# Optimization experiments

Hardware: AMD Instinct MI355X
Metric: run time of the kernel (lower is better)

The kernel has to match this reference:

```python
import jax, jax.numpy as jnp
import numpy as np
from jax import lax

EPS = 1e-5  # BatchNorm eps (inference mode: running_mean=m, running_var=v)
DN = ('NCDHW', 'OIDHW', 'NCDHW')


def _conv_bn_relu(x, W, b, g, bt, m, v, pad):
    y = lax.conv_general_dilated(x, W, window_strides=(1, 1, 1), padding=pad,
                                 dimension_numbers=DN)
    y = y + b[None, :, None, None, None]
    scale = g / jnp.sqrt(v + EPS)
    y = (y - m[None, :, None, None, None]) * scale[None, :, None, None, None] \
        + bt[None, :, None, None, None]
    return jax.nn.relu(y)


def _cal_patt(k, q, v):
    # spatial non-local attention over H*W, independently per (n, c, d)
    N, C, D, H, W = q.shape
    qf = q.reshape(N, C, D, H * W)
    kf = k.reshape(N, C, D, H * W)
    vf = v.reshape(N, C, D, H * W)
    # sigma[n,c,d,i,j] = q_i * k_j ; softmax over j ; out[j] = sum_i v_i * r_ij
    sigma = qf[..., :, None] * kf[..., None, :]          # [N,C,D,HW,HW]
    r = jax.nn.softmax(sigma, axis=-1)
    out = jnp.einsum('ncdi,ncdij->ncdj', vf, r)
    return out.reshape(N, C, D, H, W)


def _cal_datt(k, q, v):
    # temporal non-local attention over D, independently per (n, c, h, w)
    N, C, D, H, W = q.shape
    qf = jnp.transpose(q, (0, 1, 3, 4, 2))               # [N,C,H,W,D]
    kf = jnp.transpose(k, (0, 1, 3, 4, 2))
    vf = jnp.transpose(v, (0, 1, 3, 4, 2))
    sigma = qf[..., :, None] * kf[..., None, :]          # [N,C,H,W,D,D]
    r = jax.nn.softmax(sigma, axis=-1)
    out = jnp.einsum('nchwi,nchwij->nchwj', vf, r)
    return jnp.transpose(out, (0, 1, 4, 2, 3))           # back to [N,C,D,H,W]


def setup_inputs() -> dict:
    key = jax.random.key(0)
    ks = jax.random.split(key, 8)
    C, Cc = 512, 64  # features_, features_//compress
    N, D, H, W = 2, 8, 16, 16
    f32 = jnp.float32

    def bn(c):
        return (jnp.ones((c,), f32), jnp.zeros((c,), f32),
                jnp.zeros((c,), f32), jnp.ones((c,), f32))

    x = jax.random.normal(ks[0], (N, C, D, H, W), f32)
    Wq = jax.random.normal(ks[1], (Cc, C, 1, 1, 1), f32) * 0.04
    Wk = jax.random.normal(ks[2], (Cc, C, 1, 1, 1), f32) * 0.04
    Wv = jax.random.normal(ks[3], (Cc, C, 1, 1, 1), f32) * 0.04
    Ws = jax.random.normal(ks[4], (C, Cc, 3, 3, 3), f32) * 0.02
    Wd = jax.random.normal(ks[5], (C, Cc, 3, 3, 3), f32) * 0.02
    gq, btq, mq, vq = bn(Cc)
    gk, btk, mk, vk = bn(Cc)
    gv, btv, mv, vv = bn(Cc)
    gs, bts, ms, vs = bn(C)
    gd, btd, md, vd = bn(C)
    return dict(
        x=x, gama=jnp.float32(0.5),
        Wq=Wq, bq=jnp.zeros((Cc,), f32), gq=gq, btq=btq, mq=mq, vq=vq,
        Wk=Wk, bk=jnp.zeros((Cc,), f32), gk=gk, btk=btk, mk=mk, vk=vk,
        Wv=Wv, bv=jnp.zeros((Cc,), f32), gv=gv, btv=btv, mv=mv, vv=vv,
        Ws=Ws, bs=jnp.zeros((C,), f32), gs=gs, bts=bts, ms=ms, vs=vs,
        Wd=Wd, bd=jnp.zeros((C,), f32), gd=gd, btd=btd, md=md, vd=vd,
    )


def reference(x, gama,
              Wq, bq, gq, btq, mq, vq,
              Wk, bk, gk, btk, mk, vk,
              Wv, bv, gv, btv, mv, vv,
              Ws, bs, gs, bts, ms, vs,
              Wd, bd, gd, btd, md, vd):
    P0 = [(0, 0)] * 3
    P1 = [(1, 1)] * 3
    v_x = _conv_bn_relu(x, Wv, bv, gv, btv, mv, vv, P0)
    k_x = _conv_bn_relu(x, Wk, bk, gk, btk, mk, vk, P0)
    q_x = _conv_bn_relu(x, Wq, bq, gq, btq, mq, vq, P0)
    # name == 'st': both spatial and temporal attention branches
    Patt = _cal_patt(k_x, q_x, v_x)
    Patt_c = _conv_bn_relu(Patt, Ws, bs, gs, bts, ms, vs, P1)
    Datt = _cal_datt(k_x, q_x, v_x)
    Datt_c = _conv_bn_relu(Datt, Wd, bd, gd, btd, md, vd, P1)
    return gama * (Datt_c + Patt_c) + x
```

## Files before the change

### kernel.cpp

```cpp
#include <hip/hip_runtime.h>
#include <cmath>

#define EPSBN 1e-5f

namespace {
constexpr int C_IN = 512;
constexpr int CC   = 64;
constexpr int CD   = 8;
constexpr int HW   = 256;
constexpr int DHW  = CD * HW;
constexpr int QSZ  = 2 * CC * DHW;

constexpr int PG    = 18 * 18;
constexpr int GPLN  = PG * 8;
constexpr int PADSZ = 2 * 10 * 8 * GPLN;
constexpr int WTSZ  = 27 * 512 * 64;
constexpr float LOG2E = 1.44269504088896f;

typedef __attribute__((ext_vector_type(8))) short bf16x8;
typedef __attribute__((ext_vector_type(4))) float f32x4;
typedef __attribute__((ext_vector_type(16))) float f32x16;

typedef unsigned int u32_g __attribute__((address_space(1)));
typedef unsigned int u32_l __attribute__((address_space(3)));

__device__ inline unsigned short f2bf(float f) {
    unsigned u = __float_as_uint(f);
    return (unsigned short)((u + 0x7fffu + ((u >> 16) & 1u)) >> 16);
}
}

__global__ __launch_bounds__(256) void prep_small_kernel(
    const float* __restrict__ Wq, const float* __restrict__ Wk,
    const float* __restrict__ Wv, unsigned short* __restrict__ Wqkv,
    uint4* __restrict__ pads)
{
    int bid = blockIdx.x;
    int t = threadIdx.x;
    if (bid < 192) {
        int co = bid;
        const float* W = co < 64 ? Wq : co < 128 ? Wk : Wv;
        int c = co & 63;
        for (int ci = t; ci < 512; ci += 256)
            Wqkv[(size_t)co * 512 + ci] = f2bf(W[(size_t)c * 512 + ci]);
    } else {
        pads[(bid - 192) * 256 + t] = make_uint4(0, 0, 0, 0);
    }
}

__global__ __launch_bounds__(256) void qkv_gemm_kernel(
    const float* __restrict__ x, const unsigned short* __restrict__ Wqkv,
    const float* __restrict__ bq, const float* __restrict__ gq,
    const float* __restrict__ btq, const float* __restrict__ mq,
    const float* __restrict__ vq,
    const float* __restrict__ bk, const float* __restrict__ gk,
    const float* __restrict__ btk, const float* __restrict__ mk,
    const float* __restrict__ vk,
    const float* __restrict__ bv, const float* __restrict__ gv,
    const float* __restrict__ btv, const float* __restrict__ mv,
    const float* __restrict__ vv,
    float* __restrict__ outq, float* __restrict__ outk, float* __restrict__ outv)
{
    int bid = blockIdx.x;
    int n = bid >> 7, p0 = (bid & 127) * 16;

    __shared__ __align__(16) unsigned short xs[16 * 512];
    int t = threadIdx.x;

    const float* xb = x + ((size_t)n * C_IN) * DHW + p0;
#pragma unroll
    for (int pass = 0; pass < 8; ++pass) {
        int idx = pass * 256 + t;
        int ci = idx >> 2, pq = idx & 3;
        float4 v4 = *reinterpret_cast<const float4*>(xb + (size_t)ci * DHW + pq * 4);
        float arr[4] = {v4.x, v4.y, v4.z, v4.w};
#pragma unroll
        for (int u = 0; u < 4; ++u) {
            int pos = pq * 4 + u;
            int boff = pos * 1024 + ((ci * 2) ^ ((pos & 7) << 4));
            *reinterpret_cast<unsigned short*>(
                reinterpret_cast<char*>(xs) + boff) = f2bf(arr[u]);
        }
    }
    __syncthreads();

    int wid = t >> 6, lane = t & 63;
    int l15 = lane & 15, l4 = lane >> 4;
    int mh = wid * 3;
    int pos = l15;

    bf16x8 bfr[16];
    const char* xsb = reinterpret_cast<const char*>(xs) + pos * 1024;
    int swz = (pos & 7) << 4;
#pragma unroll
    for (int kk = 0; kk < 16; ++kk)
        bfr[kk] = *reinterpret_cast<const bf16x8*>(xsb + ((kk * 64 + l4 * 16) ^ swz));

    f32x4 acc[3];
#pragma unroll
    for (int i = 0; i < 3; ++i) acc[i] = (f32x4){0.f, 0.f, 0.f, 0.f};

#pragma unroll
    for (int i = 0; i < 3; ++i) {
        const unsigned short* wrow =
            Wqkv + ((size_t)(mh + i) * 16 + l15) * 512 + l4 * 8;
#pragma unroll
        for (int kk = 0; kk < 16; ++kk) {
            bf16x8 af = *reinterpret_cast<const bf16x8*>(wrow + kk * 32);
            acc[i] = __builtin_amdgcn_mfma_f32_16x16x32_bf16(af, bfr[kk], acc[i], 0, 0, 0);
        }
    }

#pragma unroll
    for (int i = 0; i < 3; ++i) {
        int mf = mh + i;
        int br = mf >> 2;
        const float* bb  = br == 0 ? bq  : br == 1 ? bk  : bv;
        const float* gg  = br == 0 ? gq  : br == 1 ? gk  : gv;
        const float* bt  = br == 0 ? btq : br == 1 ? btk : btv;
        const float* mm  = br == 0 ? mq  : br == 1 ? mk  : mv;
        const float* vvp = br == 0 ? vq  : br == 1 ? vk  : vv;
        float*       op  = br == 0 ? outq : br == 1 ? outk : outv;
        int cb = (mf & 3) * 16 + l4 * 4;
#pragma unroll
        for (int r = 0; r < 4; ++r) {
            int c = cb + r;
            float s = gg[c] * rsqrtf(vvp[c] + EPSBN);
            float val = (acc[i][r] + bb[c] - mm[c]) * s + bt[c];
            op[((size_t)(n * CC + c)) * DHW + p0 + pos] = fmaxf(val, 0.f);
        }
    }
}

__global__ __launch_bounds__(256) void att_kernel(
    const float* __restrict__ q, const float* __restrict__ k,
    const float* __restrict__ v,
    const float* __restrict__ Ws, const float* __restrict__ Wd,
    const float* __restrict__ bs, const float* __restrict__ gs,
    const float* __restrict__ bts, const float* __restrict__ ms,
    const float* __restrict__ vs,
    const float* __restrict__ bd, const float* __restrict__ gd,
    const float* __restrict__ btd, const float* __restrict__ md,
    const float* __restrict__ vd,
    unsigned short* __restrict__ Pp, unsigned short* __restrict__ Dp,
    unsigned short* __restrict__ Wt, float2* __restrict__ BNc)
{
    __shared__ __align__(16) float sk[256], sq2[256], sw[256];
    __shared__ float red[4];
    int t = threadIdx.x;
    int bid = blockIdx.x;

    if (bid < 1024) {
        int n = bid >> 9, c = (bid >> 3) & 63, d = bid & 7;
        size_t base = (size_t)bid * HW;
        float kt = k[base + t];
        float qt = q[base + t];
        float vt = v[base + t];
        float qt2 = qt * LOG2E;
        sk[t]  = kt;
        sq2[t] = qt2;

        float m = kt;
#pragma unroll
        for (int off = 32; off >= 1; off >>= 1)
            m = fmaxf(m, __shfl_xor(m, off));
        if ((t & 63) == 0) red[t >> 6] = m;
        __syncthreads();
        float kmax = fmaxf(fmaxf(red[0], red[1]), fmaxf(red[2], red[3]));

        float qkm2 = qt2 * kmax;
        float d0 = 0.f, d1 = 0.f, d2 = 0.f, d3 = 0.f;
        const float4* sk4 = reinterpret_cast<const float4*>(sk);
#pragma unroll 8
        for (int j = 0; j < 64; ++j) {
            float4 kk = sk4[j];
            d0 += __builtin_amdgcn_exp2f(fmaf(qt2, kk.x, -qkm2));
            d1 += __builtin_amdgcn_exp2f(fmaf(qt2, kk.y, -qkm2));
            d2 += __builtin_amdgcn_exp2f(fmaf(qt2, kk.z, -qkm2));
            d3 += __builtin_amdgcn_exp2f(fmaf(qt2, kk.w, -qkm2));
        }
        float den = (d0 + d1) + (d2 + d3);
        sw[t] = vt / den;
        __syncthreads();

        float kjm = kt - kmax;
        float o0 = 0.f, o1 = 0.f, o2 = 0.f, o3 = 0.f;
        const float4* sw4 = reinterpret_cast<const float4*>(sw);
        const float4* sq4 = reinterpret_cast<const float4*>(sq2);
#pragma unroll 8
        for (int i = 0; i < 64; ++i) {
            float4 ww = sw4[i];
            float4 qq = sq4[i];
            o0 += ww.x * __builtin_amdgcn_exp2f(qq.x * kjm);
            o1 += ww.y * __builtin_amdgcn_exp2f(qq.y * kjm);
            o2 += ww.z * __builtin_amdgcn_exp2f(qq.z * kjm);
            o3 += ww.w * __builtin_amdgcn_exp2f(qq.w * kjm);
        }
        float o = (o0 + o1) + (o2 + o3);

        int h = t >> 4, w = t & 15;
        size_t dst = ((((size_t)(n * 10 + d + 1) * 8 + (c >> 3)) * PG)
                      + (h + 1) * 18 + (w + 1)) * 8 + (c & 7);
        Pp[dst] = f2bf(o);
    } else if (bid < 1152) {
        int g = (bid - 1024) * 256 + t;
        int nc = g >> 8, hw = g & 255;
        int n = nc >> 6, c = nc & 63;
        size_t base = (size_t)nc * DHW + hw;

        float qv[8], kv[8], vv_[8];
#pragma unroll
        for (int d = 0; d < 8; ++d) {
            qv[d]  = q[base + d * HW];
            kv[d]  = k[base + d * HW];
            vv_[d] = v[base + d * HW];
        }
        float kmax = 0.f;
#pragma unroll
        for (int d = 0; d < 8; ++d) kmax = fmaxf(kmax, kv[d]);

        float wgt[8];
#pragma unroll
        for (int i = 0; i < 8; ++i) {
            float den = 0.f, qkm = qv[i] * kmax;
#pragma unroll
            for (int j = 0; j < 8; ++j)
                den += __expf(fmaf(qv[i], kv[j], -qkm));
            wgt[i] = vv_[i] / den;
        }
        int h = hw >> 4, w = hw & 15;
#pragma unroll
        for (int j = 0; j < 8; ++j) {
            float o = 0.f, kjm = kv[j] - kmax;
#pragma unroll
            for (int i = 0; i < 8; ++i)
                o += wgt[i] * __expf(qv[i] * kjm);
            size_t dst = ((((size_t)(n * 10 + j + 1) * 8 + (c >> 3)) * PG)
                          + (h + 1) * 18 + (w + 1)) * 8 + (c & 7);
            Dp[dst] = f2bf(o);
        }
    } else if (bid < 2176) {
        int b2 = bid - 1152;
        int b  = b2 >> 9;
        int co = b2 & 511;
        const float* W = b ? Wd : Ws;
        int cog = co >> 6, co_l = co & 63;
        int r  = co_l & 31, hi = co_l >> 5;
        unsigned short* o = Wt + (size_t)b * WTSZ;
        for (int k2 = t; k2 < 27 * 64; k2 += 256) {
            int ci  = k2 / 27;
            int tap = k2 - ci * 27;
            int kd = tap / 9, tapk = tap - kd * 9;
            int half = ci >> 5, cl = ci & 31;
            int cig = cl >> 4, ci16 = cl & 15;
            int ks = ci16 >> 3;
            float w = W[(size_t)co * 1728 + k2];
            int chunk = ((cog * 2 + half) * 3 + kd) * 2 + cig;
            int pg = (r * 2 + ks) ^ (r & 7);
            o[(size_t)chunk * 9216 + tapk * 1024 + hi * 512
              + pg * 8 + (ci16 & 7)] = f2bf(w);
        }
    } else {
        int gid = (bid - 2176) * 256 + t;
        if (gid < 1024) {
            int br = gid >> 9, co = gid & 511;
            float s, o;
            if (br == 0) {
                s = gs[co] * rsqrtf(vs[co] + EPSBN);
                o = (bs[co] - ms[co]) * s + bts[co];
            } else {
                s = gd[co] * rsqrtf(vd[co] + EPSBN);
                o = (bd[co] - md[co]) * s + btd[co];
            }
            BNc[gid] = make_float2(s, o);
        }
    }
}

__global__ __launch_bounds__(256, 1) void conv_fused_kernel(
    const unsigned short* __restrict__ Pp, const unsigned short* __restrict__ Dp,
    const unsigned short* __restrict__ Wt,
    const float2* __restrict__ BNc,
    const float* __restrict__ x, const float* __restrict__ gama,
    float* __restrict__ out)
{
    int bid = blockIdx.x;
    int cog = bid & 7;
    int pgb = (bid >> 3) & 1;
    int sl  = bid >> 4;
    int n = sl >> 3, d = sl & 7;

    __shared__ __align__(16) unsigned short lds_in[24 * 1536];
    __shared__ __align__(16) unsigned short lds_w[2 * 18432];

    int t = threadIdx.x;
    int wid = t >> 6, lane = t & 63;
    int ph = wid & 1, br = wid >> 1;
    int col  = lane & 31;
    int wcol = lane & 15;
    int hl   = (lane >> 4) & 1;
    int ks   = lane >> 5;
    int gA   = ((col * 2 + ks) ^ (col & 7)) * 8;

    f32x16 acc[2][2];
#pragma unroll
    for (int m = 0; m < 2; ++m)
#pragma unroll
        for (int p = 0; p < 2; ++p)
#pragma unroll
            for (int r = 0; r < 16; ++r)
                acc[m][p][r] = 0.f;

#define ISTAGE(hf_) do {                                                      \
    _Pragma("unroll")                                                         \
    for (int pc = 0; pc < 24; ++pc) {                                         \
        const unsigned short* sb = ((pc >= 12) ? Dp : Pp)                     \
            + ((size_t)((n * 10 + d + ((pc % 12) >> 2)) * 8 + (hf_) * 4       \
                        + ((pc % 12) & 3))) * GPLN + pgb * 1152;              \
        _Pragma("unroll")                                                     \
        for (int j = 0; j < 3; ++j) {                                         \
            if (((pc * 3 + j) & 3) == wid)                                    \
                __builtin_amdgcn_global_load_lds(                             \
                    (const u32_g*)(sb + j * 512 + lane * 8),                  \
                    (u32_l*)(lds_in + pc * 1536 + j * 512), 16, 0, 0);        \
        }                                                                     \
    }                                                                         \
} while (0)

#define DMAW(c_) do {                                                         \
    const int ch_ = (((cog * 2 + ((c_) / 6)) * 3 + (((c_) % 6) >> 1)) * 2     \
                     + ((c_) & 1)) * 9216;                                    \
    _Pragma("unroll")                                                         \
    for (int j = 0; j < 9; ++j) {                                             \
        int base = j * 2048 + wid * 512;                                      \
        const unsigned short* s0 = (base < 9216)                              \
            ? (Wt + ch_ + base)                                               \
            : (Wt + WTSZ + ch_ + (base - 9216));                              \
        __builtin_amdgcn_global_load_lds(                                     \
            (const u32_g*)(s0 + lane * 8),                                    \
            (u32_l*)(lds_w + ((c_) & 1) * 18432 + base), 16, 0, 0);           \
    }                                                                         \
} while (0)

#define COMPUTE(c_) do {                                                      \
    const int kd_ = ((c_) % 6) >> 1, cig_ = (c_) & 1;                         \
    const unsigned short* wb_ = lds_w + ((c_) & 1) * 18432 + br * 9216;       \
    const unsigned short* bp_ = lds_in + br * (12 * 1536)                     \
                                + (kd_ * 4 + cig_ * 2 + ks) * 1536;           \
    _Pragma("unroll")                                                         \
    for (int tapk = 0; tapk < 9; ++tapk) {                                    \
        const int kh_ = tapk / 3, kw_ = tapk % 3;                             \
        bf16x8 a0 = *(const bf16x8*)(wb_ + tapk * 1024 + gA);                 \
        bf16x8 a1 = *(const bf16x8*)(wb_ + tapk * 1024 + 512 + gA);           \
        bf16x8 b0 = *(const bf16x8*)(bp_ + ((ph * 4 + hl + kh_) * 18          \
                                     + wcol + kw_) * 8);                      \
        bf16x8 b1 = *(const bf16x8*)(bp_ + ((ph * 4 + 2 + hl + kh_) * 18      \
                                     + wcol + kw_) * 8);                      \
        acc[0][0] = __builtin_amdgcn_mfma_f32_32x32x16_bf16(a0, b0,           \
                        acc[0][0], 0, 0, 0);                                  \
        acc[0][1] = __builtin_amdgcn_mfma_f32_32x32x16_bf16(a0, b1,           \
                        acc[0][1], 0, 0, 0);                                  \
        acc[1][0] = __builtin_amdgcn_mfma_f32_32x32x16_bf16(a1, b0,           \
                        acc[1][0], 0, 0, 0);                                  \
        acc[1][1] = __builtin_amdgcn_mfma_f32_32x32x16_bf16(a1, b1,           \
                        acc[1][1], 0, 0, 0);                                  \
    }                                                                         \
} while (0)

    ISTAGE(0);
    DMAW(0);
    __syncthreads();

#pragma unroll
    for (int c = 0; c < 12; ++c) {
        if (c < 11) DMAW(c + 1);
        COMPUTE(c);
        __syncthreads();
        if (c == 5) {
            ISTAGE(1);
            __syncthreads();
        }
    }

#undef ISTAGE
#undef DMAW
#undef COMPUTE

    float gm = gama[0];
    float* ep = reinterpret_cast<float*>(lds_w);

    if (br == 0) {
#pragma unroll
        for (int m = 0; m < 2; ++m)
#pragma unroll
            for (int p = 0; p < 2; ++p)
#pragma unroll
                for (int r = 0; r < 16; ++r) {
                    int row = (r & 3) + 8 * (r >> 2) + 4 * ks;
                    float2 c2 = BNc[cog * 64 + m * 32 + row];
                    float v = fmaxf(acc[m][p][r] * c2.x + c2.y, 0.f);
                    ep[ph * 4096 + (m * 32 + row) * 64 + p * 32 + col] = v;
                }
    }
    __syncthreads();
    if (br == 1) {
#pragma unroll
        for (int m = 0; m < 2; ++m)
#pragma unroll
            for (int p = 0; p < 2; ++p)
#pragma unroll
                for (int r = 0; r < 16; ++r) {
                    int row = (r & 3) + 8 * (r >> 2) + 4 * ks;
                    int co = cog * 64 + m * 32 + row;
                    float2 c2 = BNc[512 + co];
                    float rd = fmaxf(acc[m][p][r] * c2.x + c2.y, 0.f);
                    float rp = ep[ph * 4096 + (m * 32 + row) * 64 + p * 32 + col];
                    int pos = pgb * 128 + ph * 64 + p * 32 + col;
                    size_t oi = ((size_t)(n * 512 + co)) * 2048 + d * 256 + pos;
                    out[oi] = gm * (rp + rd) + x[oi];
                }
    }
}

extern "C" void kernel_launch(void* const* d_in, const int* in_sizes, int n_in,
                              void* d_out, int out_size, void* d_ws, size_t ws_size,
                              hipStream_t stream)
{
    const float* x    = (const float*)d_in[0];
    const float* gama = (const float*)d_in[1];
    const float* Wq  = (const float*)d_in[2];
    const float* bq  = (const float*)d_in[3];
    const float* gq  = (const float*)d_in[4];
    const float* btq = (const float*)d_in[5];
    const float* mq  = (const float*)d_in[6];
    const float* vq  = (const float*)d_in[7];
    const float* Wk  = (const float*)d_in[8];
    const float* bk  = (const float*)d_in[9];
    const float* gk  = (const float*)d_in[10];
    const float* btk = (const float*)d_in[11];
    const float* mk  = (const float*)d_in[12];
    const float* vk  = (const float*)d_in[13];
    const float* Wv  = (const float*)d_in[14];
    const float* bv  = (const float*)d_in[15];
    const float* gv  = (const float*)d_in[16];
    const float* btv = (const float*)d_in[17];
    const float* mv  = (const float*)d_in[18];
    const float* vv  = (const float*)d_in[19];
    const float* Ws  = (const float*)d_in[20];
    const float* bs  = (const float*)d_in[21];
    const float* gs  = (const float*)d_in[22];
    const float* bts = (const float*)d_in[23];
    const float* ms  = (const float*)d_in[24];
    const float* vs  = (const float*)d_in[25];
    const float* Wd  = (const float*)d_in[26];
    const float* bd  = (const float*)d_in[27];
    const float* gd  = (const float*)d_in[28];
    const float* btd = (const float*)d_in[29];
    const float* md  = (const float*)d_in[30];
    const float* vd  = (const float*)d_in[31];

    char* ws = (char*)d_ws;
    unsigned short* Pp   = (unsigned short*)ws;
    unsigned short* Dp   = Pp + PADSZ;
    unsigned short* Wt   = Dp + PADSZ;
    unsigned short* Wqkv = Wt + 2 * WTSZ;
    float* q = (float*)(ws + 5394432);
    float* k = q + QSZ;
    float* v = k + QSZ;
    float2* BNc = (float2*)(ws + 5394432 + 3 * 1048576);

    prep_small_kernel<<<597, 256, 0, stream>>>(Wq, Wk, Wv, Wqkv, (uint4*)Pp);

    qkv_gemm_kernel<<<256, 256, 0, stream>>>(
        x, Wqkv,
        bq, gq, btq, mq, vq,
        bk, gk, btk, mk, vk,
        bv, gv, btv, mv, vv,
        q, k, v);

    att_kernel<<<2180, 256, 0, stream>>>(
        q, k, v,
        Ws, Wd,
        bs, gs, bts, ms, vs,
        bd, gd, btd, md, vd,
        Pp, Dp, Wt, BNc);

    conv_fused_kernel<<<256, 256, 0, stream>>>(
        Pp, Dp, Wt, BNc,
        x, gama, (float*)d_out);
}
```

Measured before the change: 66.11 us.

## Vectorize conv weight repack and replace syncthreads with fine-grained vmcnt waits

The Ws/Wd repack in the attention kernel now goes one block per destination chunk, with each thread writing 8 contiguous bf16 values as one 16-byte store. This cuts the repack from 1024 blocks to 192. The conv main loop drops the full __syncthreads after each step and uses raw s_barrier plus an s_waitcnt vmcnt(9), so the next weight DMA can stay in flight while the current chunk is computed. The hardcoded vmcnt count depends on how many loads DMAW issues, so a wrong count could race.

Result: faster. 59.82 us, median of 2 (-9.5%).

```diff
diff --git a/kernel.cpp b/kernel.cpp
--- a/kernel.cpp
+++ b/kernel.cpp
@@ -239,29 +239,44 @@
                           + (h + 1) * 18 + (w + 1)) * 8 + (c & 7);
             Dp[dst] = f2bf(o);
         }
-    } else if (bid < 2176) {
-        int b2 = bid - 1152;
-        int b  = b2 >> 9;
-        int co = b2 & 511;
+    } else if (bid < 1344) {
+        int u = bid - 1152;
+        int b = u / 96, chunk = u - b * 96;
         const float* W = b ? Wd : Ws;
-        int cog = co >> 6, co_l = co & 63;
-        int r  = co_l & 31, hi = co_l >> 5;
-        unsigned short* o = Wt + (size_t)b * WTSZ;
-        for (int k2 = t; k2 < 27 * 64; k2 += 256) {
-            int ci  = k2 / 27;
-            int tap = k2 - ci * 27;
-            int kd = tap / 9, tapk = tap - kd * 9;
-            int half = ci >> 5, cl = ci & 31;
-            int cig = cl >> 4, ci16 = cl & 15;
-            int ks = ci16 >> 3;
-            float w = W[(size_t)co * 1728 + k2];
-            int chunk = ((cog * 2 + half) * 3 + kd) * 2 + cig;
-            int pg = (r * 2 + ks) ^ (r & 7);
-            o[(size_t)chunk * 9216 + tapk * 1024 + hi * 512
-              + pg * 8 + (ci16 & 7)] = f2bf(w);
+        int cig = chunk & 1;
+        int kd  = (chunk >> 1) % 3;
+        int hc  = chunk / 6;
+        int half = hc & 1, cog = hc >> 1;
+        unsigned short* o = Wt + (size_t)b * WTSZ + (size_t)chunk * 9216;
+        int cibase0 = half * 32 + cig * 16;
+#pragma unroll
+        for (int it = 0; it < 5; ++it) {
+            int q4 = it * 256 + t;
+            if (q4 < 1152) {
+                int idx = q4 * 8;
+                int tapk = idx >> 10;
+                int rem  = idx & 1023;
+                int hi   = rem >> 9;
+                int pg   = (rem >> 3) & 63;
+                int r2 = (pg >> 3) & 1;
+                int r1 = ((pg >> 2) & 1) ^ r2;
+                int r0 = ((pg >> 1) & 1) ^ r1;
+                int ks = (pg & 1) ^ r0;
+                int r  = ((pg >> 3) << 2) | (r1 << 1) | r0;
+                int co = cog * 64 + hi * 32 + r;
+                int tap = kd * 9 + tapk;
+                const float* src = W + (size_t)co * 1728
+                                     + (size_t)(cibase0 + ks * 8) * 27 + tap;
+                unsigned short v8[8];
+#pragma unroll
+                for (int cin = 0; cin < 8; ++cin)
+                    v8[cin] = f2bf(src[cin * 27]);
+                *reinterpret_cast<uint4*>(o + idx) =
+                    *reinterpret_cast<const uint4*>(v8);
+            }
         }
     } else {
-        int gid = (bid - 2176) * 256 + t;
+        int gid = (bid - 1344) * 256 + t;
         if (gid < 1024) {
             int br = gid >> 9, co = gid & 511;
             float s, o;
@@ -369,16 +384,23 @@
 
     ISTAGE(0);
     DMAW(0);
-    __syncthreads();
 
 #pragma unroll
     for (int c = 0; c < 12; ++c) {
-        if (c < 11) DMAW(c + 1);
+        if (c > 0)
+            __builtin_amdgcn_s_barrier();
+        if (c < 11) {
+            DMAW(c + 1);
+            asm volatile("s_waitcnt vmcnt(9)" ::: "memory");
+        } else {
+            asm volatile("s_waitcnt vmcnt(0)" ::: "memory");
+        }
+        __builtin_amdgcn_s_barrier();
+        __builtin_amdgcn_sched_barrier(0);
         COMPUTE(c);
-        __syncthreads();
         if (c == 5) {
+            __builtin_amdgcn_s_barrier();
             ISTAGE(1);
-            __syncthreads();
         }
     }
 
@@ -398,8 +420,8 @@
                 for (int r = 0; r < 16; ++r) {
                     int row = (r & 3) + 8 * (r >> 2) + 4 * ks;
                     float2 c2 = BNc[cog * 64 + m * 32 + row];
-                    float v = fmaxf(acc[m][p][r] * c2.x + c2.y, 0.f);
-                    ep[ph * 4096 + (m * 32 + row) * 64 + p * 32 + col] = v;
+                    float v2 = fmaxf(acc[m][p][r] * c2.x + c2.y, 0.f);
+                    ep[ph * 4096 + (m * 32 + row) * 64 + p * 32 + col] = v2;
                 }
     }
     __syncthreads();
@@ -478,7 +500,7 @@
         bv, gv, btv, mv, vv,
         q, k, v);
 
-    att_kernel<<<2180, 256, 0, stream>>>(
+    att_kernel<<<1348, 256, 0, stream>>>(
         q, k, v,
         Ws, Wd,
         bs, gs, bts, ms, vs,
```
